# Performance work log

Hardware: AMD Instinct MI355X
Metric: run time of the kernel (lower is better)

The kernel has to match this reference:

```python
import jax, jax.numpy as jnp
import numpy as np

SIGMA = 0.15
POS_W, ANG_W, WID_W, SCORE_W = 1.0, 1.0, 1.0, 0.5


def setup_inputs() -> dict:
    N, MAXC = 262144, 32
    rng = np.random.default_rng(0)
    counts = rng.integers(0, MAXC, size=N)
    M = int(counts.sum())
    key = jax.random.key(0)
    k1, k2, k3 = jax.random.split(key, 3)
    pred = jax.random.normal(k1, (N, 6), jnp.float32)
    gt = jax.random.normal(k2, (M, 6), jnp.float32)
    # GT score is a BCE target: keep it in [0, 1)
    gt = gt.at[:, 5].set(jax.random.uniform(k3, (M,), jnp.float32))
    return {
        "pred": pred,
        "all_gt_grasps": gt,
        "gt_counts": jnp.asarray(counts, jnp.int32),
    }


def reference(pred, all_gt_grasps, gt_counts):
    N = pred.shape[0]
    M = all_gt_grasps.shape[0]
    # CSR-style ragged layout: segment id of each GT row
    seg = jnp.repeat(jnp.arange(N), gt_counts, total_repeat_length=M)  # (M,)
    has_gt = gt_counts > 0                                             # (N,)

    # Step 1: squared distance from each GT to its prediction's center
    ppos = pred[seg, :2]                                               # (M,2)
    sq_dist = jnp.sum((ppos - all_gt_grasps[:, :2]) ** 2, axis=1)      # (M,)

    # Step 2: Gaussian tolerance position loss (per-segment max response)
    resp = jnp.exp(-sq_dist / (2.0 * SIGMA ** 2))
    max_resp = jax.ops.segment_max(resp, seg, num_segments=N)
    loss_pos = jnp.where(has_gt, 1.0 - max_resp, 0.0)

    # Step 3: nearest GT per prediction (first argmin, matching torch.argmin)
    seg_min = jax.ops.segment_min(sq_dist, seg, num_segments=N)
    cand = jnp.where(sq_dist == seg_min[seg], jnp.arange(M), M)
    nearest = jax.ops.segment_min(cand, seg, num_segments=N)
    nearest = jnp.where(has_gt, jnp.minimum(nearest, M - 1), 0)
    ng = all_gt_grasps[nearest]                                        # (N,6)

    # Step 4: angle (L1 on cos/sin), width (smooth L1), score (BCE-with-logits)
    loss_angle = jnp.where(
        has_gt,
        jnp.abs(pred[:, 2] - ng[:, 2]) + jnp.abs(pred[:, 3] - ng[:, 3]),
        0.0,
    )
    d = pred[:, 4] - ng[:, 4]
    ad = jnp.abs(d)
    smooth_l1 = jnp.where(ad < 1.0, 0.5 * d * d, ad - 0.5)
    loss_width = jnp.where(has_gt, smooth_l1, 0.0)

    x, t = pred[:, 5], ng[:, 5]
    bce = jnp.maximum(x, 0.0) - x * t + jnp.log1p(jnp.exp(-jnp.abs(x)))
    loss_score = jnp.where(has_gt & (t > 0), bce, 0.0)

    lp = loss_pos.mean()
    la = loss_angle.mean()
    lw = loss_width.mean()
    ls = loss_score.mean()
    lg = POS_W * lp + ANG_W * la + WID_W * lw + SCORE_W * ls
    return jnp.stack([lp, la, lw, ls, lg])
```

## Files before the change

kernel.cpp:

```cpp
#include <hip/hip_runtime.h>
#include <math.h>
#include <float.h>

#define BS 256
#define MAXC 31
#define MAXGT (BS * MAXC)
typedef unsigned long long u64;
typedef unsigned short u16;


__global__ void block_sum_kernel(const int* __restrict__ counts,
                                 int* __restrict__ blockSums, int N) {
    int i = blockIdx.x * BS + threadIdx.x;
    int v = (i < N) ? counts[i] : 0;
    for (int o = 32; o > 0; o >>= 1) v += __shfl_down(v, o, 64);
    __shared__ int ws[BS / 64];
    int lane = threadIdx.x & 63, w = threadIdx.x >> 6;
    if (lane == 0) ws[w] = v;
    __syncthreads();
    if (threadIdx.x == 0) {
        int s = 0;
        for (int ww = 0; ww < BS / 64; ++ww) s += ws[ww];
        blockSums[blockIdx.x] = s;
    }
}

__global__ void scan_kernel(const int* __restrict__ blockSums,
                            int* __restrict__ blockOffsets, int nb) {
    __shared__ int tmp[1024];
    int t = threadIdx.x;
    int v = (t < nb) ? blockSums[t] : 0;
    tmp[t] = v;
    __syncthreads();
    for (int off = 1; off < 1024; off <<= 1) {
        int x = (t >= off) ? tmp[t - off] : 0;
        __syncthreads();
        tmp[t] += x;
        __syncthreads();
    }
    if (t < nb) blockOffsets[t] = tmp[t] - v;
}

__global__ void __launch_bounds__(BS)
fused_kernel(const float* __restrict__ pred, const float* __restrict__ gt,
             const int* __restrict__ counts, const int* __restrict__ blockOffsets,
             float4* __restrict__ partials, int N) {
    const int t = threadIdx.x;
    const int b = blockIdx.x;
    const int i = b * BS + t;
    const int lane = t & 63, w = t >> 6;

    __shared__ u16 ownerMap[MAXGT];
    __shared__ float2 pxy[BS];
    __shared__ u64 bestLds[BS];
    __shared__ int waveTot[BS / 64];
    __shared__ int sTotal;
    __shared__ float red[BS / 64][4];

    const int c = (i < N) ? counts[i] : 0;
    int incl = c;
    for (int o = 1; o < 64; o <<= 1) {
        int x = __shfl_up(incl, o, 64);
        if (lane >= o) incl += x;
    }
    if (lane == 63) waveTot[w] = incl;
    __syncthreads();
    int wbase = 0;
    for (int ww = 0; ww < w; ++ww) wbase += waveTot[ww];
    const int localStart = wbase + incl - c;
    if (t == BS - 1) sTotal = localStart + c;
    bestLds[t] = ~0ULL;
    if (i < N) pxy[t] = reinterpret_cast<const float2*>(pred)[(size_t)i * 3];
    for (int j = 0; j < c; ++j) ownerMap[localStart + j] = (u16)t;
    __syncthreads();

    const int base = blockOffsets[b];
    const int blockTotal = sTotal;
    const float2* gxy = reinterpret_cast<const float2*>(gt);

    for (int tile = 0; tile < blockTotal; tile += BS * 4) {
        int j[4]; float2 g[4]; bool valid[4];
#pragma unroll
        for (int u = 0; u < 4; ++u) {
            j[u] = tile + u * BS + t;
            valid[u] = j[u] < blockTotal;
            if (valid[u]) g[u] = gxy[(size_t)(base + j[u]) * 3];
        }
#pragma unroll
        for (int u = 0; u < 4; ++u) {
            if (valid[u]) {
                const int owner = (int)ownerMap[j[u]];
                const float2 p = pxy[owner];
                const float dx = p.x - g[u].x, dy = p.y - g[u].y;
                const float d2 = dx * dx + dy * dy;
                const u64 key = ((u64)__float_as_uint(d2) << 32)
                              | (unsigned int)(base + j[u]);
                atomicMin(&bestLds[owner], key);
            }
        }
    }
    __syncthreads();

    float lp = 0.f, la = 0.f, lw = 0.f, ls = 0.f;
    if (i < N && c > 0) {
        const u64 key = bestLds[t];
        const float d2 = __uint_as_float((unsigned int)(key >> 32));
        const int bj = (int)(key & 0xffffffffu);
        lp = 1.0f - expf(-d2 / 0.045f);

        const float* p = pred + (size_t)i * 6;
        const float2 p23 = *reinterpret_cast<const float2*>(p + 2);
        const float2 p45 = *reinterpret_cast<const float2*>(p + 4);
        const float* ng = gt + (size_t)bj * 6;
        const float2 g23 = *reinterpret_cast<const float2*>(ng + 2);
        const float2 g45 = *reinterpret_cast<const float2*>(ng + 4);

        la = fabsf(p23.x - g23.x) + fabsf(p23.y - g23.y);
        const float d = p45.x - g45.x;
        const float ad = fabsf(d);
        lw = (ad < 1.0f) ? 0.5f * d * d : ad - 0.5f;
        const float x = p45.y;
        if (g45.y > 0.0f) {
            ls = fmaxf(x, 0.0f) - x * g45.y + log1pf(expf(-fabsf(x)));
        }
    }

    for (int o = 32; o > 0; o >>= 1) {
        lp += __shfl_down(lp, o, 64);
        la += __shfl_down(la, o, 64);
        lw += __shfl_down(lw, o, 64);
        ls += __shfl_down(ls, o, 64);
    }
    if (lane == 0) { red[w][0] = lp; red[w][1] = la; red[w][2] = lw; red[w][3] = ls; }
    __syncthreads();
    if (t == 0) {
        float s0 = 0, s1 = 0, s2 = 0, s3 = 0;
        for (int ww = 0; ww < BS / 64; ++ww) {
            s0 += red[ww][0]; s1 += red[ww][1]; s2 += red[ww][2]; s3 += red[ww][3];
        }
        partials[b] = make_float4(s0, s1, s2, s3);
    }
}

__global__ void finalize_kernel(const float4* __restrict__ partials,
                                float* __restrict__ out, int nb, int N) {
    const int t = threadIdx.x;
    const int lane = t & 63, w = t >> 6;
    double s0 = 0, s1 = 0, s2 = 0, s3 = 0;
    if (t < nb) {
        const float4 v = partials[t];
        s0 = v.x; s1 = v.y; s2 = v.z; s3 = v.w;
    }
    for (int o = 32; o > 0; o >>= 1) {
        s0 += __shfl_down(s0, o, 64);
        s1 += __shfl_down(s1, o, 64);
        s2 += __shfl_down(s2, o, 64);
        s3 += __shfl_down(s3, o, 64);
    }
    __shared__ double red[16][4];
    if (lane == 0) { red[w][0] = s0; red[w][1] = s1; red[w][2] = s2; red[w][3] = s3; }
    __syncthreads();
    if (t == 0) {
        double t0 = 0, t1 = 0, t2 = 0, t3 = 0;
        for (int ww = 0; ww < blockDim.x / 64; ++ww) {
            t0 += red[ww][0]; t1 += red[ww][1]; t2 += red[ww][2]; t3 += red[ww][3];
        }
        const double inv = 1.0 / (double)N;
        const float lp = (float)(t0 * inv);
        const float la = (float)(t1 * inv);
        const float lw = (float)(t2 * inv);
        const float ls = (float)(t3 * inv);
        out[0] = lp; out[1] = la; out[2] = lw; out[3] = ls;
        out[4] = lp + la + lw + 0.5f * ls;
    }
}

extern "C" void kernel_launch(void* const* d_in, const int* in_sizes, int n_in,
                              void* d_out, int out_size, void* d_ws, size_t ws_size,
                              hipStream_t stream) {
    const float* pred = (const float*)d_in[0];
    const float* gt = (const float*)d_in[1];
    const int* counts = (const int*)d_in[2];
    float* out = (float*)d_out;

    const int N = in_sizes[2];
    const int numBlocks = (N + BS - 1) / BS;

    int* blockSums = (int*)d_ws;
    int* blockOffsets = (int*)((char*)d_ws + 4096);
    float4* partials = (float4*)((char*)d_ws + 8192);

    block_sum_kernel<<<numBlocks, BS, 0, stream>>>(counts, blockSums, N);
    scan_kernel<<<1, 1024, 0, stream>>>(blockSums, blockOffsets, numBlocks);
    fused_kernel<<<numBlocks, BS, 0, stream>>>(pred, gt, counts, blockOffsets,
                                               partials, N);
    finalize_kernel<<<1, 1024, 0, stream>>>(partials, out, numBlocks, N);
}
```

Before: 166.1 us.

## Fuse block-sum, scan, main pass and finalize into one kernel with global flags

Replaces the four-kernel pipeline with a single kernel. Each block publishes its GT count, and the last block to arrive computes the exclusive scan and writes per-block offsets to a state array that the other blocks spin on. The last block to finish reduces all partial sums and writes the final losses. This removes three kernel launches and their serial gaps, at the cost of a memset, spin-waiting, and a dependence on all 1024 blocks being co-resident, which could deadlock if they are not.

```diff
diff --git a/kernel.cpp b/kernel.cpp
--- a/kernel.cpp
+++ b/kernel.cpp
@@ -7,46 +7,17 @@
 #define MAXGT (BS * MAXC)
 typedef unsigned long long u64;
 typedef unsigned short u16;
-
-
-__global__ void block_sum_kernel(const int* __restrict__ counts,
-                                 int* __restrict__ blockSums, int N) {
-    int i = blockIdx.x * BS + threadIdx.x;
-    int v = (i < N) ? counts[i] : 0;
-    for (int o = 32; o > 0; o >>= 1) v += __shfl_down(v, o, 64);
-    __shared__ int ws[BS / 64];
-    int lane = threadIdx.x & 63, w = threadIdx.x >> 6;
-    if (lane == 0) ws[w] = v;
-    __syncthreads();
-    if (threadIdx.x == 0) {
-        int s = 0;
-        for (int ww = 0; ww < BS / 64; ++ww) s += ws[ww];
-        blockSums[blockIdx.x] = s;
-    }
-}
-
-__global__ void scan_kernel(const int* __restrict__ blockSums,
-                            int* __restrict__ blockOffsets, int nb) {
-    __shared__ int tmp[1024];
-    int t = threadIdx.x;
-    int v = (t < nb) ? blockSums[t] : 0;
-    tmp[t] = v;
-    __syncthreads();
-    for (int off = 1; off < 1024; off <<= 1) {
-        int x = (t >= off) ? tmp[t - off] : 0;
-        __syncthreads();
-        tmp[t] += x;
-        __syncthreads();
-    }
-    if (t < nb) blockOffsets[t] = tmp[t] - v;
-}
-
-__global__ void __launch_bounds__(BS)
-fused_kernel(const float* __restrict__ pred, const float* __restrict__ gt,
-             const int* __restrict__ counts, const int* __restrict__ blockOffsets,
-             float4* __restrict__ partials, int N) {
+typedef unsigned int u32;
+
+
+__global__ void __launch_bounds__(BS, 4)
+fused_all(const float* __restrict__ pred, const float* __restrict__ gt,
+          const int* __restrict__ counts,
+          u32* arrived, u32* done, u64* state, u32* blockSums,
+          float* partials, float* out, int N) {
     const int t = threadIdx.x;
     const int b = blockIdx.x;
+    const int nb = gridDim.x;
     const int i = b * BS + t;
     const int lane = t & 63, w = t >> 6;
 
@@ -55,7 +26,10 @@
     __shared__ u64 bestLds[BS];
     __shared__ int waveTot[BS / 64];
     __shared__ int sTotal;
+    __shared__ int sBase;
+    __shared__ int sFlag;
     __shared__ float red[BS / 64][4];
+    __shared__ double dred[BS / 64][4];
 
     const int c = (i < N) ? counts[i] : 0;
     int incl = c;
@@ -68,13 +42,56 @@
     int wbase = 0;
     for (int ww = 0; ww < w; ++ww) wbase += waveTot[ww];
     const int localStart = wbase + incl - c;
-    if (t == BS - 1) sTotal = localStart + c;
+
+    if (t == BS - 1) {
+        const int tot = localStart + c;
+        sTotal = tot;
+        atomicExch(&blockSums[b], (u32)tot);
+        __threadfence();
+        const u32 old = atomicAdd(arrived, 1u);
+        sFlag = (old == (u32)(nb - 1)) ? 1 : 0;
+    }
+
     bestLds[t] = ~0ULL;
     if (i < N) pxy[t] = reinterpret_cast<const float2*>(pred)[(size_t)i * 3];
     for (int j = 0; j < c; ++j) ownerMap[localStart + j] = (u16)t;
     __syncthreads();
 
-    const int base = blockOffsets[b];
+    if (sFlag) {
+        __threadfence();
+        if (t < 64) {
+            const int bi = t * 16;
+            u32 v[16];
+            int s = 0;
+#pragma unroll
+            for (int k = 0; k < 16; ++k) {
+                v[k] = atomicAdd(&blockSums[bi + k], 0u);
+                s += (int)v[k];
+            }
+            int isc = s;
+            for (int o = 1; o < 64; o <<= 1) {
+                int x = __shfl_up(isc, o, 64);
+                if (t >= o) isc += x;
+            }
+            int excl = isc - s;
+#pragma unroll
+            for (int k = 0; k < 16; ++k) {
+                if (bi + k == b) sBase = excl;
+                atomicExch(&state[bi + k], (1ULL << 32) | (u64)(u32)excl);
+                excl += (int)v[k];
+            }
+        }
+    } else {
+        if (t == 0) {
+            u64 st;
+            while (((st = atomicAdd(&state[b], 0ULL)) >> 32) == 0ULL)
+                __builtin_amdgcn_s_sleep(2);
+            sBase = (int)(u32)st;
+        }
+    }
+    __syncthreads();
+
+    const int base = sBase;
     const int blockTotal = sTotal;
     const float2* gxy = reinterpret_cast<const float2*>(gt);
 
@@ -94,7 +111,7 @@
                 const float dx = p.x - g[u].x, dy = p.y - g[u].y;
                 const float d2 = dx * dx + dy * dy;
                 const u64 key = ((u64)__float_as_uint(d2) << 32)
-                              | (unsigned int)(base + j[u]);
+                              | (u32)(base + j[u]);
                 atomicMin(&bestLds[owner], key);
             }
         }
@@ -104,7 +121,7 @@
     float lp = 0.f, la = 0.f, lw = 0.f, ls = 0.f;
     if (i < N && c > 0) {
         const u64 key = bestLds[t];
-        const float d2 = __uint_as_float((unsigned int)(key >> 32));
+        const float d2 = __uint_as_float((u32)(key >> 32));
         const int bj = (int)(key & 0xffffffffu);
         lp = 1.0f - expf(-d2 / 0.045f);
 
@@ -138,40 +155,46 @@
         for (int ww = 0; ww < BS / 64; ++ww) {
             s0 += red[ww][0]; s1 += red[ww][1]; s2 += red[ww][2]; s3 += red[ww][3];
         }
-        partials[b] = make_float4(s0, s1, s2, s3);
-    }
-}
-
-__global__ void finalize_kernel(const float4* __restrict__ partials,
-                                float* __restrict__ out, int nb, int N) {
-    const int t = threadIdx.x;
-    const int lane = t & 63, w = t >> 6;
-    double s0 = 0, s1 = 0, s2 = 0, s3 = 0;
-    if (t < nb) {
-        const float4 v = partials[t];
-        s0 = v.x; s1 = v.y; s2 = v.z; s3 = v.w;
-    }
-    for (int o = 32; o > 0; o >>= 1) {
-        s0 += __shfl_down(s0, o, 64);
-        s1 += __shfl_down(s1, o, 64);
-        s2 += __shfl_down(s2, o, 64);
-        s3 += __shfl_down(s3, o, 64);
-    }
-    __shared__ double red[16][4];
-    if (lane == 0) { red[w][0] = s0; red[w][1] = s1; red[w][2] = s2; red[w][3] = s3; }
-    __syncthreads();
-    if (t == 0) {
-        double t0 = 0, t1 = 0, t2 = 0, t3 = 0;
-        for (int ww = 0; ww < blockDim.x / 64; ++ww) {
-            t0 += red[ww][0]; t1 += red[ww][1]; t2 += red[ww][2]; t3 += red[ww][3];
-        }
-        const double inv = 1.0 / (double)N;
-        const float lp = (float)(t0 * inv);
-        const float la = (float)(t1 * inv);
-        const float lw = (float)(t2 * inv);
-        const float ls = (float)(t3 * inv);
-        out[0] = lp; out[1] = la; out[2] = lw; out[3] = ls;
-        out[4] = lp + la + lw + 0.5f * ls;
+        atomicExch(&partials[b * 4 + 0], s0);
+        atomicExch(&partials[b * 4 + 1], s1);
+        atomicExch(&partials[b * 4 + 2], s2);
+        atomicExch(&partials[b * 4 + 3], s3);
+        __threadfence();
+        const u32 old = atomicAdd(done, 1u);
+        sFlag = (old == (u32)(nb - 1)) ? 1 : 0;
+    }
+    __syncthreads();
+
+    if (sFlag) {
+        __threadfence();
+        double a0 = 0, a1 = 0, a2 = 0, a3 = 0;
+        for (int r = t; r < nb; r += BS) {
+            a0 += (double)atomicAdd(&partials[r * 4 + 0], 0.0f);
+            a1 += (double)atomicAdd(&partials[r * 4 + 1], 0.0f);
+            a2 += (double)atomicAdd(&partials[r * 4 + 2], 0.0f);
+            a3 += (double)atomicAdd(&partials[r * 4 + 3], 0.0f);
+        }
+        for (int o = 32; o > 0; o >>= 1) {
+            a0 += __shfl_down(a0, o, 64);
+            a1 += __shfl_down(a1, o, 64);
+            a2 += __shfl_down(a2, o, 64);
+            a3 += __shfl_down(a3, o, 64);
+        }
+        if (lane == 0) { dred[w][0] = a0; dred[w][1] = a1; dred[w][2] = a2; dred[w][3] = a3; }
+        __syncthreads();
+        if (t == 0) {
+            double t0 = 0, t1 = 0, t2 = 0, t3 = 0;
+            for (int ww = 0; ww < BS / 64; ++ww) {
+                t0 += dred[ww][0]; t1 += dred[ww][1]; t2 += dred[ww][2]; t3 += dred[ww][3];
+            }
+            const double inv = 1.0 / (double)N;
+            const float flp = (float)(t0 * inv);
+            const float fla = (float)(t1 * inv);
+            const float flw = (float)(t2 * inv);
+            const float fls = (float)(t3 * inv);
+            out[0] = flp; out[1] = fla; out[2] = flw; out[3] = fls;
+            out[4] = flp + fla + flw + 0.5f * fls;
+        }
     }
 }
 
@@ -186,13 +209,14 @@
     const int N = in_sizes[2];
     const int numBlocks = (N + BS - 1) / BS;
 
-    int* blockSums = (int*)d_ws;
-    int* blockOffsets = (int*)((char*)d_ws + 4096);
-    float4* partials = (float4*)((char*)d_ws + 8192);
-
-    block_sum_kernel<<<numBlocks, BS, 0, stream>>>(counts, blockSums, N);
-    scan_kernel<<<1, 1024, 0, stream>>>(blockSums, blockOffsets, numBlocks);
-    fused_kernel<<<numBlocks, BS, 0, stream>>>(pred, gt, counts, blockOffsets,
-                                               partials, N);
-    finalize_kernel<<<1, 1024, 0, stream>>>(partials, out, numBlocks, N);
+    char* ws = (char*)d_ws;
+    u32* arrived = (u32*)ws;
+    u32* done = (u32*)(ws + 4);
+    u64* state = (u64*)(ws + 64);
+    u32* blockSums = (u32*)(ws + 12288);
+    float* partials = (float*)(ws + 16384);
+
+    hipMemsetAsync(d_ws, 0, 64 + (size_t)numBlocks * sizeof(u64), stream);
+    fused_all<<<numBlocks, BS, 0, stream>>>(pred, gt, counts, arrived, done,
+                                            state, blockSums, partials, out, N);
 }
```

Result: slower. 233.8 us (+40.8%).

## Replace LDS atomicMin owner-map scan with per-thread segment loop over staged chunks

Applied to the files above, without the earlier changes.

Instead of having each thread process GT rows and combine results with 64-bit LDS atomicMin keyed by an owner map, GT xy coordinates are staged cooperatively into an LDS chunk. Each thread then loops serially over its own segment and keeps a running min and argmin in registers. This removes the atomics and the ownerMap construction, at the cost of load imbalance across threads (segments of 0 to 31 rows) and extra barriers per chunk. A strict less-than comparison keeps the first-argmin semantics.

```diff
diff --git a/kernel.cpp b/kernel.cpp
--- a/kernel.cpp
+++ b/kernel.cpp
@@ -3,10 +3,8 @@
 #include <float.h>
 
 #define BS 256
-#define MAXC 31
-#define MAXGT (BS * MAXC)
+#define CHUNK 2048
 typedef unsigned long long u64;
-typedef unsigned short u16;
 
 
 __global__ void block_sum_kernel(const int* __restrict__ counts,
@@ -50,9 +48,7 @@
     const int i = b * BS + t;
     const int lane = t & 63, w = t >> 6;
 
-    __shared__ u16 ownerMap[MAXGT];
-    __shared__ float2 pxy[BS];
-    __shared__ u64 bestLds[BS];
+    __shared__ float2 chunkXY[CHUNK];
     __shared__ int waveTot[BS / 64];
     __shared__ int sTotal;
     __shared__ float red[BS / 64][4];
@@ -67,51 +63,50 @@
     __syncthreads();
     int wbase = 0;
     for (int ww = 0; ww < w; ++ww) wbase += waveTot[ww];
-    const int localStart = wbase + incl - c;
-    if (t == BS - 1) sTotal = localStart + c;
-    bestLds[t] = ~0ULL;
-    if (i < N) pxy[t] = reinterpret_cast<const float2*>(pred)[(size_t)i * 3];
-    for (int j = 0; j < c; ++j) ownerMap[localStart + j] = (u16)t;
+    const int myStart = wbase + incl - c;
+    const int myEnd = myStart + c;
+    if (t == BS - 1) sTotal = myEnd;
     __syncthreads();
 
     const int base = blockOffsets[b];
     const int blockTotal = sTotal;
     const float2* gxy = reinterpret_cast<const float2*>(gt);
 
-    for (int tile = 0; tile < blockTotal; tile += BS * 4) {
-        int j[4]; float2 g[4]; bool valid[4];
+    const float2 myp = (i < N)
+        ? reinterpret_cast<const float2*>(pred)[(size_t)i * 3]
+        : make_float2(0.f, 0.f);
+
+    float best = FLT_MAX;
+    int bestRow = 0;
+
+    for (int chunkLo = 0; chunkLo < blockTotal; chunkLo += CHUNK) {
 #pragma unroll
-        for (int u = 0; u < 4; ++u) {
-            j[u] = tile + u * BS + t;
-            valid[u] = j[u] < blockTotal;
-            if (valid[u]) g[u] = gxy[(size_t)(base + j[u]) * 3];
+        for (int u = 0; u < CHUNK / BS; ++u) {
+            const int j = u * BS + t;
+            const int gj = chunkLo + j;
+            if (gj < blockTotal) chunkXY[j] = gxy[(size_t)(base + gj) * 3];
         }
-#pragma unroll
-        for (int u = 0; u < 4; ++u) {
-            if (valid[u]) {
-                const int owner = (int)ownerMap[j[u]];
-                const float2 p = pxy[owner];
-                const float dx = p.x - g[u].x, dy = p.y - g[u].y;
-                const float d2 = dx * dx + dy * dy;
-                const u64 key = ((u64)__float_as_uint(d2) << 32)
-                              | (unsigned int)(base + j[u]);
-                atomicMin(&bestLds[owner], key);
-            }
+        __syncthreads();
+        const int lo = myStart > chunkLo ? myStart : chunkLo;
+        const int hiLim = chunkLo + CHUNK;
+        const int hi = myEnd < hiLim ? myEnd : hiLim;
+        for (int j = lo; j < hi; ++j) {
+            const float2 g = chunkXY[j - chunkLo];
+            const float dx = myp.x - g.x, dy = myp.y - g.y;
+            const float d2 = dx * dx + dy * dy;
+            if (d2 < best) { best = d2; bestRow = base + j; }
         }
+        __syncthreads();
     }
-    __syncthreads();
 
     float lp = 0.f, la = 0.f, lw = 0.f, ls = 0.f;
     if (i < N && c > 0) {
-        const u64 key = bestLds[t];
-        const float d2 = __uint_as_float((unsigned int)(key >> 32));
-        const int bj = (int)(key & 0xffffffffu);
-        lp = 1.0f - expf(-d2 / 0.045f);
+        lp = 1.0f - expf(-best / 0.045f);
 
         const float* p = pred + (size_t)i * 6;
         const float2 p23 = *reinterpret_cast<const float2*>(p + 2);
         const float2 p45 = *reinterpret_cast<const float2*>(p + 4);
-        const float* ng = gt + (size_t)bj * 6;
+        const float* ng = gt + (size_t)bestRow * 6;
         const float2 g23 = *reinterpret_cast<const float2*>(ng + 2);
         const float2 g45 = *reinterpret_cast<const float2*>(ng + 4);
 
```

New measurement: 168.6 us. No clear change (+1.5%).
